# Kernel optimization log

Measured on AMD Instinct MI355X. Metric: run time of the kernel, lower is better.

## Reference

```python
import jax, jax.numpy as jnp
import numpy as np

B, N, FIN, D1, D2 = 4096, 64, 256, 512, 128
NEG = -10000000.0


def setup_inputs() -> dict:
    key = jax.random.key(0)
    ks = jax.random.split(key, 12)
    s = lambda fan_in: 1.0 / np.sqrt(fan_in)
    return {
        "obs_x": jax.random.normal(ks[0], (B, FIN), jnp.float32),
        "others": jax.random.normal(ks[1], (B, N, FIN), jnp.float32),
        "action_mask": jax.random.randint(ks[2], (B, D2), 0, 2, jnp.int32),
        "W1": jax.random.normal(ks[3], (FIN, D1), jnp.float32) * s(FIN),
        "b1": jnp.zeros((D1,), jnp.float32),
        "W2": jax.random.normal(ks[4], (2 * D1, D2), jnp.float32) * s(2 * D1),
        "b2": jnp.zeros((D2,), jnp.float32),
        "W3": jax.random.normal(ks[5], (2 * D1, D2), jnp.float32) * s(2 * D1),
        "b3": jnp.zeros((D2,), jnp.float32),
        "W4": jax.random.normal(ks[6], (D2, 1), jnp.float32) * s(D2),
        "b4": jnp.zeros((1,), jnp.float32),
    }


def reference(obs_x, others, action_mask, W1, b1, W2, b2, W3, b3, W4, b4):
    # shared fc1 projection of self obs and other agents' obs
    x = obs_x @ W1 + b1                       # [B, D1]
    y = jnp.einsum("bnf,fd->bnd", others, W1) + b1  # [B, N, D1]
    # single-query dot-product attention over other agents
    alpha = jnp.einsum("bd,bnd->bn", x, y) / jnp.sqrt(jnp.float32(x.shape[-1]))
    beta = jax.nn.softmax(alpha, axis=-1)     # [B, N]
    c = jnp.einsum("bn,bnd->bd", beta, y)     # context [B, D1]
    out = jnp.concatenate([x, c], axis=-1)    # [B, 2*D1]
    out1 = jax.nn.softmax(out @ W2 + b2, axis=-1)  # policy branch (softmax then mask, as in source)
    mask = action_mask.astype(out1.dtype)
    logits = out1 + NEG * (1.0 - mask)
    value = (out @ W3 + b3) @ W4 + b4         # [B, 1] value head (stored as self._value_out)
    del value  # forward() returns only the masked logits
    return logits.reshape(-1, D2)
```

## Files before the change

### kernel.cpp

```cpp
#include <hip/hip_runtime.h>
#include <hip/hip_bf16.h>


typedef unsigned short u16;
typedef __bf16 bf16x8 __attribute__((ext_vector_type(8)));
typedef float f32x4 __attribute__((ext_vector_type(4)));

#define FIN 256
#define D1  512
#define D2  128
#define NNA 64
#define NEGV -10000000.0f

__device__ __forceinline__ float bf2f(u16 u) {
  unsigned int i = ((unsigned int)u) << 16;
  return __builtin_bit_cast(float, i);
}
__device__ __forceinline__ u16 f2bf(float f) {
  unsigned int i = __builtin_bit_cast(unsigned int, f);
  return (u16)((i + 0x7FFFu + ((i >> 16) & 1u)) >> 16);
}
__device__ __forceinline__ bf16x8 ld_frag_g(const u16* p) {
  return __builtin_bit_cast(bf16x8, *(const uint4*)p);
}
__device__ __forceinline__ bf16x8 ld_frag_f32(const float* p) {
  float4 a = *(const float4*)p, b = *(const float4*)(p + 4);
  u16 s[8];
  s[0] = f2bf(a.x); s[1] = f2bf(a.y); s[2] = f2bf(a.z); s[3] = f2bf(a.w);
  s[4] = f2bf(b.x); s[5] = f2bf(b.y); s[6] = f2bf(b.z); s[7] = f2bf(b.w);
  return __builtin_bit_cast(bf16x8, *(uint4*)s);
}

__global__ __launch_bounds__(256) void k_prep(const float* __restrict__ W1,
                                              const float* __restrict__ W2,
                                              u16* __restrict__ W1p,
                                              u16* __restrict__ W2p,
                                              u16* __restrict__ W1tp) {
  int tid = blockIdx.x * 256 + threadIdx.x;
  if (tid < 131072) {
    int idx = tid;
    int j = idx & 7, lane = (idx >> 3) & 63, nt = (idx >> 9) & 31, kt = idx >> 14;
    int k = kt * 32 + (lane >> 4) * 8 + j;
    int n = nt * 16 + (lane & 15);
    W1p[idx] = f2bf(W1[k * D1 + n]);
  } else if (tid < 163840) {
    int idx = tid - 131072;
    int j = idx & 7, lane = (idx >> 3) & 63, nt = (idx >> 9) & 7, kt = idx >> 12;
    int k = kt * 32 + (lane >> 4) * 8 + j;
    int n = nt * 16 + (lane & 15);
    W2p[idx] = f2bf(W2[k * D2 + n]);
  } else {
    int idx = tid - 163840;
    int j = idx & 7, lane = (idx >> 3) & 63, nt = (idx >> 9) & 15, kt = idx >> 13;
    int k = kt * 32 + (lane >> 4) * 8 + j;
    int n = nt * 16 + (lane & 15);
    W1tp[idx] = f2bf(W1[n * D1 + k]);
  }
}

__global__ __launch_bounds__(256) void k_x(const float* __restrict__ obs,
                                           const u16* __restrict__ W1p,
                                           const float* __restrict__ pb1,
                                           u16* __restrict__ outw) {
  const int w = threadIdx.x >> 6, lane = threadIdx.x & 63;
  const int q = lane >> 4, c0 = lane & 15;
  const int m0 = blockIdx.x * 128 + w * 32;
  const int ntg0 = blockIdx.y * 8;

  f32x4 acc[2][8];
#pragma unroll
  for (int a = 0; a < 2; ++a)
#pragma unroll
    for (int c = 0; c < 8; ++c) acc[a][c] = (f32x4){0.f, 0.f, 0.f, 0.f};

#pragma unroll 1
  for (int kt = 0; kt < 8; ++kt) {
    bf16x8 afr[2], bfr[8];
#pragma unroll
    for (int mt = 0; mt < 2; ++mt)
      afr[mt] = ld_frag_f32(obs + (m0 + mt * 16 + c0) * FIN + kt * 32 + q * 8);
#pragma unroll
    for (int nt = 0; nt < 8; ++nt)
      bfr[nt] = ld_frag_g(W1p + ((kt * 32 + ntg0 + nt) * 64 + lane) * 8);
#pragma unroll
    for (int mt = 0; mt < 2; ++mt)
#pragma unroll
      for (int nt = 0; nt < 8; ++nt)
        acc[mt][nt] = __builtin_amdgcn_mfma_f32_16x16x32_bf16(afr[mt], bfr[nt], acc[mt][nt], 0, 0, 0);
  }

#pragma unroll
  for (int nt = 0; nt < 8; ++nt) {
    const int n = (ntg0 + nt) * 16 + c0;
    const float bias = pb1[n];
#pragma unroll
    for (int mt = 0; mt < 2; ++mt)
#pragma unroll
      for (int i = 0; i < 4; ++i) {
        const int row = m0 + mt * 16 + q * 4 + i;
        outw[row * 1024 + n] = f2bf(acc[mt][nt][i] + bias);
      }
  }
}

__global__ __launch_bounds__(256) void k_z(const u16* __restrict__ outw,
                                           const u16* __restrict__ W1tp,
                                           float* __restrict__ zbuf) {
  const int w = threadIdx.x >> 6, lane = threadIdx.x & 63;
  const int q = lane >> 4, c0 = lane & 15;
  const int m0 = blockIdx.x * 128 + w * 32;
  const int ntg0 = blockIdx.y * 8;

  f32x4 acc[2][8];
#pragma unroll
  for (int a = 0; a < 2; ++a)
#pragma unroll
    for (int c = 0; c < 8; ++c) acc[a][c] = (f32x4){0.f, 0.f, 0.f, 0.f};

#pragma unroll 1
  for (int kt = 0; kt < 16; ++kt) {
    bf16x8 afr[2], bfr[8];
#pragma unroll
    for (int mt = 0; mt < 2; ++mt)
      afr[mt] = ld_frag_g(outw + (m0 + mt * 16 + c0) * 1024 + kt * 32 + q * 8);
#pragma unroll
    for (int nt = 0; nt < 8; ++nt)
      bfr[nt] = ld_frag_g(W1tp + ((kt * 16 + ntg0 + nt) * 64 + lane) * 8);
#pragma unroll
    for (int mt = 0; mt < 2; ++mt)
#pragma unroll
      for (int nt = 0; nt < 8; ++nt)
        acc[mt][nt] = __builtin_amdgcn_mfma_f32_16x16x32_bf16(afr[mt], bfr[nt], acc[mt][nt], 0, 0, 0);
  }

#pragma unroll
  for (int nt = 0; nt < 8; ++nt) {
    const int n = (ntg0 + nt) * 16 + c0;
#pragma unroll
    for (int mt = 0; mt < 2; ++mt)
#pragma unroll
      for (int i = 0; i < 4; ++i) {
        const int row = m0 + mt * 16 + q * 4 + i;
        zbuf[row * 256 + n] = acc[mt][nt][i];
      }
  }
}

__global__ __launch_bounds__(256, 4) void k_attn(const float* __restrict__ others,
                                                 const float* __restrict__ zbuf,
                                                 u16* __restrict__ obarb) {
  __shared__ float s_alpha[64];
  __shared__ float s_beta[64];
  __shared__ float s_part[1024];

  const int tid = threadIdx.x;
  const int b = blockIdx.x;
  const int w = tid >> 6, l = tid & 63;
  const float* src = others + (size_t)b * (NNA * FIN);

  const float4 z4 = *(const float4*)(zbuf + b * 256 + 4 * l);

  float4 o4[16];
#pragma unroll
  for (int r = 0; r < 16; ++r)
    o4[r] = *(const float4*)(src + (w * 16 + r) * 256 + 4 * l);

#pragma unroll
  for (int r = 0; r < 16; ++r) {
    float s = o4[r].x * z4.x + o4[r].y * z4.y + o4[r].z * z4.z + o4[r].w * z4.w;
    s += __shfl_xor(s, 1);  s += __shfl_xor(s, 2);  s += __shfl_xor(s, 4);
    s += __shfl_xor(s, 8);  s += __shfl_xor(s, 16); s += __shfl_xor(s, 32);
    if (l == r) s_alpha[w * 16 + r] = s * 0.04419417382415922f;
  }
  __syncthreads();

  if (tid < 64) {
    float v = s_alpha[tid];
    float mx = v;
#pragma unroll
    for (int off = 1; off < 64; off <<= 1) mx = fmaxf(mx, __shfl_xor(mx, off));
    float e = __expf(v - mx);
    float se = e;
#pragma unroll
    for (int off = 1; off < 64; off <<= 1) se += __shfl_xor(se, off);
    s_beta[tid] = e / se;
  }
  __syncthreads();

  float4 p = (float4){0.f, 0.f, 0.f, 0.f};
#pragma unroll
  for (int r = 0; r < 16; ++r) {
    const float bb = s_beta[w * 16 + r];
    p.x += bb * o4[r].x; p.y += bb * o4[r].y; p.z += bb * o4[r].z; p.w += bb * o4[r].w;
  }
  *(float4*)(&s_part[w * 256 + 4 * l]) = p;
  __syncthreads();

  const float v = s_part[tid] + s_part[tid + 256] + s_part[tid + 512] + s_part[tid + 768];
  obarb[(size_t)b * 256 + tid] = f2bf(v);
}

__global__ __launch_bounds__(256) void k_c(const u16* __restrict__ obarb,
                                           const u16* __restrict__ W1p,
                                           const float* __restrict__ pb1,
                                           u16* __restrict__ outw) {
  const int w = threadIdx.x >> 6, lane = threadIdx.x & 63;
  const int q = lane >> 4, c0 = lane & 15;
  const int m0 = blockIdx.x * 128 + w * 32;
  const int ntg0 = blockIdx.y * 8;

  f32x4 acc[2][8];
#pragma unroll
  for (int a = 0; a < 2; ++a)
#pragma unroll
    for (int c = 0; c < 8; ++c) acc[a][c] = (f32x4){0.f, 0.f, 0.f, 0.f};

#pragma unroll 1
  for (int kt = 0; kt < 8; ++kt) {
    bf16x8 afr[2], bfr[8];
#pragma unroll
    for (int mt = 0; mt < 2; ++mt)
      afr[mt] = ld_frag_g(obarb + (m0 + mt * 16 + c0) * 256 + kt * 32 + q * 8);
#pragma unroll
    for (int nt = 0; nt < 8; ++nt)
      bfr[nt] = ld_frag_g(W1p + ((kt * 32 + ntg0 + nt) * 64 + lane) * 8);
#pragma unroll
    for (int mt = 0; mt < 2; ++mt)
#pragma unroll
      for (int nt = 0; nt < 8; ++nt)
        acc[mt][nt] = __builtin_amdgcn_mfma_f32_16x16x32_bf16(afr[mt], bfr[nt], acc[mt][nt], 0, 0, 0);
  }

#pragma unroll
  for (int nt = 0; nt < 8; ++nt) {
    const int n = (ntg0 + nt) * 16 + c0;
    const float bias = pb1[n];
#pragma unroll
    for (int mt = 0; mt < 2; ++mt)
#pragma unroll
      for (int i = 0; i < 4; ++i) {
        const int row = m0 + mt * 16 + q * 4 + i;
        outw[row * 1024 + 512 + n] = f2bf(acc[mt][nt][i] + bias);
      }
  }
}

__global__ __launch_bounds__(64) void k_head(const u16* __restrict__ outw,
                                             const u16* __restrict__ W2p,
                                             const float* __restrict__ pb2,
                                             const int* __restrict__ mask,
                                             float* __restrict__ out) {
  const int lane = threadIdx.x & 63;
  const int q = lane >> 4, c0 = lane & 15;
  const int m0 = blockIdx.x * 16;

  f32x4 acc[8];
#pragma unroll
  for (int c = 0; c < 8; ++c) acc[c] = (f32x4){0.f, 0.f, 0.f, 0.f};

#pragma unroll 1
  for (int kt = 0; kt < 32; ++kt) {
    bf16x8 afr, bfr[8];
    afr = ld_frag_g(outw + (m0 + c0) * 1024 + kt * 32 + q * 8);
#pragma unroll
    for (int nt = 0; nt < 8; ++nt)
      bfr[nt] = ld_frag_g(W2p + ((kt * 8 + nt) * 64 + lane) * 8);
#pragma unroll
    for (int nt = 0; nt < 8; ++nt)
      acc[nt] = __builtin_amdgcn_mfma_f32_16x16x32_bf16(afr, bfr[nt], acc[nt], 0, 0, 0);
  }

  float b2f[8];
#pragma unroll
  for (int nt = 0; nt < 8; ++nt) b2f[nt] = pb2[nt * 16 + c0];

#pragma unroll
  for (int i = 0; i < 4; ++i) {
    const int row = m0 + q * 4 + i;
    float v[8];
    float mx = -3.0e38f;
#pragma unroll
    for (int nt = 0; nt < 8; ++nt) { v[nt] = acc[nt][i] + b2f[nt]; mx = fmaxf(mx, v[nt]); }
    mx = fmaxf(mx, __shfl_xor(mx, 1)); mx = fmaxf(mx, __shfl_xor(mx, 2));
    mx = fmaxf(mx, __shfl_xor(mx, 4)); mx = fmaxf(mx, __shfl_xor(mx, 8));
    float se = 0.f;
#pragma unroll
    for (int nt = 0; nt < 8; ++nt) { v[nt] = __expf(v[nt] - mx); se += v[nt]; }
    se += __shfl_xor(se, 1); se += __shfl_xor(se, 2);
    se += __shfl_xor(se, 4); se += __shfl_xor(se, 8);
    const float inv = 1.f / se;
#pragma unroll
    for (int nt = 0; nt < 8; ++nt) {
      const int col = nt * 16 + c0;
      float p = fminf(fmaxf(v[nt] * inv, 0.f), 1.f);
      float o = mask[row * D2 + col] ? p : (p + NEGV);
      out[row * D2 + col] = o;
    }
  }
}

extern "C" void kernel_launch(void* const* d_in, const int* in_sizes, int n_in,
                              void* d_out, int out_size, void* d_ws, size_t ws_size,
                              hipStream_t stream) {
  const float* obs = (const float*)d_in[0];
  const float* oth = (const float*)d_in[1];
  const int*   msk = (const int*)d_in[2];
  const float* W1  = (const float*)d_in[3];
  const float* b1  = (const float*)d_in[4];
  const float* W2  = (const float*)d_in[5];
  const float* b2  = (const float*)d_in[6];
  float* out = (float*)d_out;

  char* ws = (char*)d_ws;
  u16*   W1p   = (u16*)ws;
  u16*   W2p   = (u16*)(ws + 262144);
  u16*   W1tp  = (u16*)(ws + 327680);
  u16*   outw  = (u16*)(ws + 589824);
  float* zbuf  = (float*)(ws + 8978432);
  u16*   obarb = (u16*)(ws + 13172736);

  k_prep<<<1152, 256, 0, stream>>>(W1, W2, W1p, W2p, W1tp);
  k_x<<<dim3(32, 4), 256, 0, stream>>>(obs, W1p, b1, outw);
  k_z<<<dim3(32, 2), 256, 0, stream>>>(outw, W1tp, zbuf);
  k_attn<<<4096, 256, 0, stream>>>(oth, zbuf, obarb);
  k_c<<<dim3(32, 4), 256, 0, stream>>>(obarb, W1p, b1, outw);
  k_head<<<256, 64, 0, stream>>>(outw, W2p, b2, msk, out);
}
```

Measured before the change: 430.8 us.

## Fuse context projection into policy head kernel and shrink x/z launch blocks

Merges the context projection (obar @ W1 + b1) into the head kernel. The context rows now live in shared memory instead of being written to and reread from the global outw buffer, which shrinks to 512 columns. The head splits its 128 output columns across two waves, using a cross-wave shared-memory reduction for the softmax. k_x and k_z switch to 64-thread blocks with four times as many blocks. This removes one launch and a global round trip, but the tail kernel recomputes the context projection with only 256 blocks of 128 threads, which could lower parallelism for that GEMM.

```diff
diff --git a/kernel.cpp b/kernel.cpp
--- a/kernel.cpp
+++ b/kernel.cpp
@@ -58,13 +58,13 @@
   }
 }
 
-__global__ __launch_bounds__(256) void k_x(const float* __restrict__ obs,
-                                           const u16* __restrict__ W1p,
-                                           const float* __restrict__ pb1,
-                                           u16* __restrict__ outw) {
-  const int w = threadIdx.x >> 6, lane = threadIdx.x & 63;
+__global__ __launch_bounds__(64) void k_x(const float* __restrict__ obs,
+                                          const u16* __restrict__ W1p,
+                                          const float* __restrict__ pb1,
+                                          u16* __restrict__ outw) {
+  const int lane = threadIdx.x & 63;
   const int q = lane >> 4, c0 = lane & 15;
-  const int m0 = blockIdx.x * 128 + w * 32;
+  const int m0 = blockIdx.x * 32;
   const int ntg0 = blockIdx.y * 8;
 
   f32x4 acc[2][8];
@@ -98,17 +98,17 @@
 #pragma unroll
       for (int i = 0; i < 4; ++i) {
         const int row = m0 + mt * 16 + q * 4 + i;
-        outw[row * 1024 + n] = f2bf(acc[mt][nt][i] + bias);
+        outw[row * 512 + n] = f2bf(acc[mt][nt][i] + bias);
       }
   }
 }
 
-__global__ __launch_bounds__(256) void k_z(const u16* __restrict__ outw,
-                                           const u16* __restrict__ W1tp,
-                                           float* __restrict__ zbuf) {
-  const int w = threadIdx.x >> 6, lane = threadIdx.x & 63;
+__global__ __launch_bounds__(64) void k_z(const u16* __restrict__ outw,
+                                          const u16* __restrict__ W1tp,
+                                          float* __restrict__ zbuf) {
+  const int lane = threadIdx.x & 63;
   const int q = lane >> 4, c0 = lane & 15;
-  const int m0 = blockIdx.x * 128 + w * 32;
+  const int m0 = blockIdx.x * 32;
   const int ntg0 = blockIdx.y * 8;
 
   f32x4 acc[2][8];
@@ -122,7 +122,7 @@
     bf16x8 afr[2], bfr[8];
 #pragma unroll
     for (int mt = 0; mt < 2; ++mt)
-      afr[mt] = ld_frag_g(outw + (m0 + mt * 16 + c0) * 1024 + kt * 32 + q * 8);
+      afr[mt] = ld_frag_g(outw + (m0 + mt * 16 + c0) * 512 + kt * 32 + q * 8);
 #pragma unroll
     for (int nt = 0; nt < 8; ++nt)
       bfr[nt] = ld_frag_g(W1tp + ((kt * 16 + ntg0 + nt) * 64 + lane) * 8);
@@ -200,99 +200,116 @@
   obarb[(size_t)b * 256 + tid] = f2bf(v);
 }
 
-__global__ __launch_bounds__(256) void k_c(const u16* __restrict__ obarb,
-                                           const u16* __restrict__ W1p,
-                                           const float* __restrict__ pb1,
-                                           u16* __restrict__ outw) {
-  const int w = threadIdx.x >> 6, lane = threadIdx.x & 63;
-  const int q = lane >> 4, c0 = lane & 15;
-  const int m0 = blockIdx.x * 128 + w * 32;
-  const int ntg0 = blockIdx.y * 8;
-
-  f32x4 acc[2][8];
-#pragma unroll
-  for (int a = 0; a < 2; ++a)
-#pragma unroll
-    for (int c = 0; c < 8; ++c) acc[a][c] = (f32x4){0.f, 0.f, 0.f, 0.f};
-
-#pragma unroll 1
-  for (int kt = 0; kt < 8; ++kt) {
-    bf16x8 afr[2], bfr[8];
-#pragma unroll
-    for (int mt = 0; mt < 2; ++mt)
-      afr[mt] = ld_frag_g(obarb + (m0 + mt * 16 + c0) * 256 + kt * 32 + q * 8);
-#pragma unroll
-    for (int nt = 0; nt < 8; ++nt)
-      bfr[nt] = ld_frag_g(W1p + ((kt * 32 + ntg0 + nt) * 64 + lane) * 8);
-#pragma unroll
-    for (int mt = 0; mt < 2; ++mt)
-#pragma unroll
-      for (int nt = 0; nt < 8; ++nt)
-        acc[mt][nt] = __builtin_amdgcn_mfma_f32_16x16x32_bf16(afr[mt], bfr[nt], acc[mt][nt], 0, 0, 0);
-  }
-
-#pragma unroll
-  for (int nt = 0; nt < 8; ++nt) {
-    const int n = (ntg0 + nt) * 16 + c0;
-    const float bias = pb1[n];
-#pragma unroll
-    for (int mt = 0; mt < 2; ++mt)
-#pragma unroll
-      for (int i = 0; i < 4; ++i) {
-        const int row = m0 + mt * 16 + q * 4 + i;
-        outw[row * 1024 + 512 + n] = f2bf(acc[mt][nt][i] + bias);
-      }
-  }
-}
-
-__global__ __launch_bounds__(64) void k_head(const u16* __restrict__ outw,
-                                             const u16* __restrict__ W2p,
-                                             const float* __restrict__ pb2,
-                                             const int* __restrict__ mask,
-                                             float* __restrict__ out) {
-  const int lane = threadIdx.x & 63;
+__global__ __launch_bounds__(128) void k_tail(const u16* __restrict__ outw,
+                                              const u16* __restrict__ obarb,
+                                              const u16* __restrict__ W1p,
+                                              const float* __restrict__ pb1,
+                                              const u16* __restrict__ W2p,
+                                              const float* __restrict__ pb2,
+                                              const int* __restrict__ mask,
+                                              float* __restrict__ out) {
+  __shared__ __align__(16) u16 c_s[16 * 520];
+  __shared__ float s_mx[2][16];
+  __shared__ float s_se[2][16];
+
+  const int tid = threadIdx.x;
+  const int w = tid >> 6, lane = tid & 63;
   const int q = lane >> 4, c0 = lane & 15;
   const int m0 = blockIdx.x * 16;
 
-  f32x4 acc[8];
-#pragma unroll
-  for (int c = 0; c < 8; ++c) acc[c] = (f32x4){0.f, 0.f, 0.f, 0.f};
-
-#pragma unroll 1
-  for (int kt = 0; kt < 32; ++kt) {
-    bf16x8 afr, bfr[8];
-    afr = ld_frag_g(outw + (m0 + c0) * 1024 + kt * 32 + q * 8);
-#pragma unroll
-    for (int nt = 0; nt < 8; ++nt)
-      bfr[nt] = ld_frag_g(W2p + ((kt * 8 + nt) * 64 + lane) * 8);
-#pragma unroll
-    for (int nt = 0; nt < 8; ++nt)
+  {
+    f32x4 acc[16];
+#pragma unroll
+    for (int c = 0; c < 16; ++c) acc[c] = (f32x4){0.f, 0.f, 0.f, 0.f};
+
+#pragma unroll 1
+    for (int kt = 0; kt < 8; ++kt) {
+      bf16x8 afr = ld_frag_g(obarb + (m0 + c0) * 256 + kt * 32 + q * 8);
+      bf16x8 bfr[16];
+#pragma unroll
+      for (int nt = 0; nt < 16; ++nt)
+        bfr[nt] = ld_frag_g(W1p + ((kt * 32 + w * 16 + nt) * 64 + lane) * 8);
+#pragma unroll
+      for (int nt = 0; nt < 16; ++nt)
+        acc[nt] = __builtin_amdgcn_mfma_f32_16x16x32_bf16(afr, bfr[nt], acc[nt], 0, 0, 0);
+    }
+
+#pragma unroll
+    for (int nt = 0; nt < 16; ++nt) {
+      const int n = w * 256 + nt * 16 + c0;
+      const float bias = pb1[n];
+#pragma unroll
+      for (int i = 0; i < 4; ++i)
+        c_s[(q * 4 + i) * 520 + n] = f2bf(acc[nt][i] + bias);
+    }
+  }
+  __syncthreads();
+
+  f32x4 acc[4];
+#pragma unroll
+  for (int c = 0; c < 4; ++c) acc[c] = (f32x4){0.f, 0.f, 0.f, 0.f};
+
+#pragma unroll 1
+  for (int kt = 0; kt < 16; ++kt) {
+    bf16x8 afr = ld_frag_g(outw + (m0 + c0) * 512 + kt * 32 + q * 8);
+    bf16x8 bfr[4];
+#pragma unroll
+    for (int nt = 0; nt < 4; ++nt)
+      bfr[nt] = ld_frag_g(W2p + ((kt * 8 + w * 4 + nt) * 64 + lane) * 8);
+#pragma unroll
+    for (int nt = 0; nt < 4; ++nt)
       acc[nt] = __builtin_amdgcn_mfma_f32_16x16x32_bf16(afr, bfr[nt], acc[nt], 0, 0, 0);
   }
-
-  float b2f[8];
-#pragma unroll
-  for (int nt = 0; nt < 8; ++nt) b2f[nt] = pb2[nt * 16 + c0];
-
+#pragma unroll 1
+  for (int kt = 0; kt < 16; ++kt) {
+    bf16x8 afr = __builtin_bit_cast(bf16x8, *(const uint4*)(c_s + c0 * 520 + kt * 32 + q * 8));
+    bf16x8 bfr[4];
+#pragma unroll
+    for (int nt = 0; nt < 4; ++nt)
+      bfr[nt] = ld_frag_g(W2p + (((kt + 16) * 8 + w * 4 + nt) * 64 + lane) * 8);
+#pragma unroll
+    for (int nt = 0; nt < 4; ++nt)
+      acc[nt] = __builtin_amdgcn_mfma_f32_16x16x32_bf16(afr, bfr[nt], acc[nt], 0, 0, 0);
+  }
+
+  float b2f[4];
+#pragma unroll
+  for (int nt = 0; nt < 4; ++nt) b2f[nt] = pb2[(w * 4 + nt) * 16 + c0];
+
+  float vv[4][4];
 #pragma unroll
   for (int i = 0; i < 4; ++i) {
-    const int row = m0 + q * 4 + i;
-    float v[8];
     float mx = -3.0e38f;
 #pragma unroll
-    for (int nt = 0; nt < 8; ++nt) { v[nt] = acc[nt][i] + b2f[nt]; mx = fmaxf(mx, v[nt]); }
+    for (int nt = 0; nt < 4; ++nt) { vv[i][nt] = acc[nt][i] + b2f[nt]; mx = fmaxf(mx, vv[i][nt]); }
     mx = fmaxf(mx, __shfl_xor(mx, 1)); mx = fmaxf(mx, __shfl_xor(mx, 2));
     mx = fmaxf(mx, __shfl_xor(mx, 4)); mx = fmaxf(mx, __shfl_xor(mx, 8));
+    if (c0 == 0) s_mx[w][q * 4 + i] = mx;
+  }
+  __syncthreads();
+
+#pragma unroll
+  for (int i = 0; i < 4; ++i) {
+    const int r = q * 4 + i;
+    const float mx = fmaxf(s_mx[0][r], s_mx[1][r]);
     float se = 0.f;
 #pragma unroll
-    for (int nt = 0; nt < 8; ++nt) { v[nt] = __expf(v[nt] - mx); se += v[nt]; }
+    for (int nt = 0; nt < 4; ++nt) { vv[i][nt] = __expf(vv[i][nt] - mx); se += vv[i][nt]; }
     se += __shfl_xor(se, 1); se += __shfl_xor(se, 2);
     se += __shfl_xor(se, 4); se += __shfl_xor(se, 8);
-    const float inv = 1.f / se;
-#pragma unroll
-    for (int nt = 0; nt < 8; ++nt) {
-      const int col = nt * 16 + c0;
-      float p = fminf(fmaxf(v[nt] * inv, 0.f), 1.f);
+    if (c0 == 0) s_se[w][q * 4 + i] = se;
+  }
+  __syncthreads();
+
+#pragma unroll
+  for (int i = 0; i < 4; ++i) {
+    const int r = q * 4 + i;
+    const int row = m0 + r;
+    const float inv = 1.f / (s_se[0][r] + s_se[1][r]);
+#pragma unroll
+    for (int nt = 0; nt < 4; ++nt) {
+      const int col = (w * 4 + nt) * 16 + c0;
+      float p = fminf(fmaxf(vv[i][nt] * inv, 0.f), 1.f);
       float o = mask[row * D2 + col] ? p : (p + NEGV);
       out[row * D2 + col] = o;
     }
@@ -316,13 +333,12 @@
   u16*   W2p   = (u16*)(ws + 262144);
   u16*   W1tp  = (u16*)(ws + 327680);
   u16*   outw  = (u16*)(ws + 589824);
-  float* zbuf  = (float*)(ws + 8978432);
-  u16*   obarb = (u16*)(ws + 13172736);
+  float* zbuf  = (float*)(ws + 4784128);
+  u16*   obarb = (u16*)(ws + 8978432);
 
   k_prep<<<1152, 256, 0, stream>>>(W1, W2, W1p, W2p, W1tp);
-  k_x<<<dim3(32, 4), 256, 0, stream>>>(obs, W1p, b1, outw);
-  k_z<<<dim3(32, 2), 256, 0, stream>>>(outw, W1tp, zbuf);
+  k_x<<<dim3(128, 4), 64, 0, stream>>>(obs, W1p, b1, outw);
+  k_z<<<dim3(128, 2), 64, 0, stream>>>(outw, W1tp, zbuf);
   k_attn<<<4096, 256, 0, stream>>>(oth, zbuf, obarb);
-  k_c<<<dim3(32, 4), 256, 0, stream>>>(obarb, W1p, b1, outw);
-  k_head<<<256, 64, 0, stream>>>(outw, W2p, b2, msk, out);
-}
+  k_tail<<<256, 128, 0, stream>>>(outw, obarb, W1p, b1, W2p, b2, msk, out);
+}
```

After: 427.2 us. About the same (-0.8%).
